# Kernel tuning notes

Measured on AMD Instinct MI355X. Metric: run time of the kernel, lower is better.

Reference implementation:

```python
import jax, jax.numpy as jnp
import numpy as np

H = 1024   # lstm_size
Z = 512    # z_size
E = 32     # subseq_embedding_dim
B = 256    # batch
T = 64     # length


def setup_inputs() -> dict:
    key = jax.random.key(0)
    ks = jax.random.split(key, 16)
    k = 1.0 / np.sqrt(H)  # PyTorch default uniform init bound
    u = lambda kk, shape: jax.random.uniform(kk, shape, jnp.float32, -k, k)
    return {
        "z": jax.random.normal(ks[0], (1, B, Z), jnp.float32),
        "targets": jax.random.normal(ks[1], (T, B, E), jnp.float32),
        "length": T,
        # LSTM layer 0 (input E -> H), gate order i,f,g,o as in PyTorch
        "W_ih0": u(ks[2], (4 * H, E)), "W_hh0": u(ks[3], (4 * H, H)),
        "b_ih0": u(ks[4], (4 * H,)),   "b_hh0": u(ks[5], (4 * H,)),
        # LSTM layer 1 (input H -> H)
        "W_ih1": u(ks[6], (4 * H, H)), "W_hh1": u(ks[7], (4 * H, H)),
        "b_ih1": u(ks[8], (4 * H,)),   "b_hh1": u(ks[9], (4 * H,)),
        # per-layer z -> initial hidden projections
        "Wz0": u(ks[10], (H, Z)), "bz0": u(ks[11], (H,)),
        "Wz1": u(ks[12], (H, Z)), "bz1": u(ks[13], (H,)),
        # output projection H -> E
        "Wp": u(ks[14], (E, H)), "bp": u(ks[15], (E,)),
    }


def _lstm_cell(x, h, c, W_ih, W_hh, b_ih, b_hh):
    # gates: [i, f, g, o] stacked along last dim (PyTorch layout)
    g = x @ W_ih.T + h @ W_hh.T + (b_ih + b_hh)
    i, f, gg, o = jnp.split(g, 4, axis=-1)
    c2 = jax.nn.sigmoid(f) * c + jax.nn.sigmoid(i) * jnp.tanh(gg)
    h2 = jax.nn.sigmoid(o) * jnp.tanh(c2)
    return h2, c2


def reference(z, targets, length, W_ih0, W_hh0, b_ih0, b_hh0,
              W_ih1, W_hh1, b_ih1, b_hh1, Wz0, bz0, Wz1, bz1, Wp, bp):
    batch = z.shape[1]
    emb = targets.shape[-1]
    z0 = z[0]  # (B, Z)
    # initial hidden = tanh(Linear(z)) per layer, initial cell = zeros
    h0 = jnp.tanh(z0 @ Wz0.T + bz0)
    h1 = jnp.tanh(z0 @ Wz1.T + bz1)
    c0 = jnp.zeros_like(h0)
    c1 = jnp.zeros_like(h1)

    # teacher-forced inputs: step 0 is zeros, step t uses targets[t-1] (detached)
    inputs = jnp.concatenate(
        [jnp.zeros((1, batch, emb), targets.dtype),
         jax.lax.stop_gradient(targets[: length - 1])], axis=0)

    def step(carry, x):
        h0, c0, h1, c1 = carry
        h0, c0 = _lstm_cell(x, h0, c0, W_ih0, W_hh0, b_ih0, b_hh0)
        h1, c1 = _lstm_cell(h0, h1, c1, W_ih1, W_hh1, b_ih1, b_hh1)
        out = h1 @ Wp.T + bp  # (B, E)
        return (h0, c0, h1, c1), out

    _, outs = jax.lax.scan(step, (h0, c0, h1, c1), inputs)
    return outs  # (length, B, E) == embedding_outputs
```

## Files before the change

### kernel.cpp

```cpp
#include <hip/hip_runtime.h>

#define TT 64
#define BB 256
#define HH 1024
#define ZZ 512
#define EE 32

#define NKB0 33
#define NKB1 64
#define NKBZ 16
#define NKBP 32

#define SLOTSH ((size_t)(HH / 16) * BB * 16)

typedef __attribute__((ext_vector_type(8))) short short8;
typedef __attribute__((ext_vector_type(4))) float f4;

__device__ __forceinline__ f4 mfma16(short8 a, short8 b, f4 c) {
  return __builtin_amdgcn_mfma_f32_16x16x32_bf16(a, b, c, 0, 0, 0);
}

__device__ __forceinline__ unsigned short f2bf(float f) {
  unsigned u = __builtin_bit_cast(unsigned, f);
  u = u + 0x7fffu + ((u >> 16) & 1u);
  return (unsigned short)(u >> 16);
}

__device__ __forceinline__ float sigm(float x) { return 1.0f / (1.0f + __expf(-x)); }
__device__ __forceinline__ float tanh_f(float x) { return 1.0f - 2.0f / (__expf(2.0f * x) + 1.0f); }

__device__ __forceinline__ short8 ld16(const short* p) { return *(const short8*)p; }

__device__ __forceinline__ short8 ld16_byp(const short* p) {
  union { unsigned long long u[2]; short8 v; } t;
  t.u[0] = __hip_atomic_load((const unsigned long long*)p, __ATOMIC_RELAXED, __HIP_MEMORY_SCOPE_AGENT);
  t.u[1] = __hip_atomic_load((const unsigned long long*)p + 1, __ATOMIC_RELAXED, __HIP_MEMORY_SCOPE_AGENT);
  return t.v;
}

__device__ __forceinline__ void st4_byp(short* p, unsigned v) {
  __hip_atomic_store((unsigned*)p, v, __ATOMIC_RELAXED, __HIP_MEMORY_SCOPE_AGENT);
}

__device__ __forceinline__ void bar_arrive(unsigned* bar, int btid, int jt, unsigned gen) {
  asm volatile("s_waitcnt vmcnt(0)" ::: "memory");
  __syncthreads();
  if (threadIdx.x == 0) {
    unsigned* base = bar + btid * (10 * 32);
    unsigned* leaf = base + (jt >> 3) * 32;
    unsigned prev = __hip_atomic_fetch_add(leaf, 1u, __ATOMIC_RELAXED, __HIP_MEMORY_SCOPE_AGENT);
    if (prev == gen * 8u - 1u) {
      unsigned rp = __hip_atomic_fetch_add(base + 8 * 32, 1u, __ATOMIC_RELAXED, __HIP_MEMORY_SCOPE_AGENT);
      if (rp == gen * 8u - 1u)
        __hip_atomic_store(base + 9 * 32, gen, __ATOMIC_RELAXED, __HIP_MEMORY_SCOPE_AGENT);
    }
  }
}

__device__ __forceinline__ void bar_wait(unsigned* bar, int btid, unsigned gen) {
  if (threadIdx.x == 0) {
    unsigned* flag = bar + btid * (10 * 32) + 9 * 32;
    while (__hip_atomic_load(flag, __ATOMIC_RELAXED, __HIP_MEMORY_SCOPE_AGENT) < gen)
      __builtin_amdgcn_s_sleep(1);
  }
  __syncthreads();
}

__global__ void pack_all(
    const float* __restrict__ z, const float* __restrict__ tg,
    const float* __restrict__ Wih0, const float* __restrict__ Whh0,
    const float* __restrict__ Wih1, const float* __restrict__ Whh1,
    const float* __restrict__ Wz0, const float* __restrict__ Wz1,
    const float* __restrict__ Wp,
    short* __restrict__ W0P, short* __restrict__ W1P,
    short* __restrict__ WzP, short* __restrict__ WpP,
    short* __restrict__ zbf, short* __restrict__ Xbf)
{
  const int N0 = 64 * NKB0 * 4 * 64;
  const int N1 = 64 * NKB1 * 4 * 64;
  const int N2 = 32 * NKBZ * 4 * 64;
  const int N3 = NKBP * 2 * 64;
  const int N4 = (BB * ZZ) / 8;
  const int N5 = (TT * BB * EE) / 8;
  const int TOT = N0 + N1 + N2 + N3 + N4 + N5;
  for (int idx = blockIdx.x * blockDim.x + threadIdx.x; idx < TOT;
       idx += gridDim.x * blockDim.x) {
    int j = idx;
    short8 ov;
    if (j < N0) {
      const int l = j & 63, fc = (j >> 6) & 3, rest = j >> 8;
      const int kb = rest % NKB0, jt = rest / NKB0;
      const int row = fc * HH + jt * 16 + (l & 15);
      const int k0 = kb * 32 + ((l >> 4) * 8);
      #pragma unroll
      for (int i = 0; i < 8; ++i) {
        const int k = k0 + i;
        const float v = (k < HH) ? Whh0[(size_t)row * HH + k]
                                 : Wih0[(size_t)row * EE + (k - HH)];
        ov[i] = (short)f2bf(v);
      }
      *(short8*)(W0P + (size_t)j * 8) = ov;
      continue;
    }
    j -= N0;
    if (j < N1) {
      const int l = j & 63, fc = (j >> 6) & 3, rest = j >> 8;
      const int kb = rest & 63, jt = rest >> 6;
      const int row = fc * HH + jt * 16 + (l & 15);
      const int k0 = kb * 32 + ((l >> 4) * 8);
      #pragma unroll
      for (int i = 0; i < 8; ++i) {
        const int k = k0 + i;
        const float v = (k < HH) ? Wih1[(size_t)row * HH + k]
                                 : Whh1[(size_t)row * HH + (k - HH)];
        ov[i] = (short)f2bf(v);
      }
      *(short8*)(W1P + (size_t)j * 8) = ov;
      continue;
    }
    j -= N1;
    if (j < N2) {
      const int l = j & 63, fc = (j >> 6) & 3, rest = j >> 8;
      const int kb = rest & 15, ct = rest >> 4;
      const int col = ct * 64 + fc * 16 + (l & 15);
      const int lay = col >> 10, ch = col & (HH - 1);
      const int k0 = kb * 32 + ((l >> 4) * 8);
      const float* W = lay ? Wz1 : Wz0;
      #pragma unroll
      for (int i = 0; i < 8; ++i) ov[i] = (short)f2bf(W[(size_t)ch * ZZ + k0 + i]);
      *(short8*)(WzP + (size_t)j * 8) = ov;
      continue;
    }
    j -= N2;
    if (j < N3) {
      const int l = j & 63, fc = (j >> 6) & 1, kb = j >> 7;
      const int e = fc * 16 + (l & 15);
      const int k0 = kb * 32 + ((l >> 4) * 8);
      #pragma unroll
      for (int i = 0; i < 8; ++i) ov[i] = (short)f2bf(Wp[(size_t)e * HH + k0 + i]);
      *(short8*)(WpP + (size_t)j * 8) = ov;
      continue;
    }
    j -= N3;
    if (j < N4) {
      #pragma unroll
      for (int i = 0; i < 8; ++i) ov[i] = (short)f2bf(z[(size_t)j * 8 + i]);
      *(short8*)(zbf + (size_t)j * 8) = ov;
      continue;
    }
    j -= N4;
    {
      const int base = j * 8;
      const int t = base >> 13, rem = base & 8191;
      if (t == 0) {
        #pragma unroll
        for (int i = 0; i < 8; ++i) ov[i] = 0;
      } else {
        #pragma unroll
        for (int i = 0; i < 8; ++i) ov[i] = (short)f2bf(tg[(size_t)(t - 1) * 8192 + rem + i]);
      }
      *(short8*)(Xbf + (size_t)j * 8) = ov;
    }
  }
}

__global__ void __launch_bounds__(256, 1)
init_h(const short* __restrict__ WzP, const short* __restrict__ zbf,
       const float* __restrict__ bz0, const float* __restrict__ bz1,
       short* __restrict__ H0s0, short* __restrict__ H1s0)
{
  __shared__ float red[2][64][66];
  const int wg = blockIdx.x;
  const int btile = (wg >> 5) * 64;
  const int ct = wg & 31;
  const int tid = threadIdx.x;
  const int wv = tid >> 6, ln = tid & 63;
  const int lr = ln & 15, lk = (ln >> 4) * 8, hi4 = (ln >> 4) * 4;

  f4 acc[4][4];
  #pragma unroll
  for (int r = 0; r < 4; ++r)
    #pragma unroll
    for (int c = 0; c < 4; ++c) acc[r][c] = (f4)0.0f;

  #pragma unroll 2
  for (int i = 0; i < 4; ++i) {
    const int kb = wv + i * 4;
    short8 av[4], bv[4];
    const short* ap = zbf + (size_t)(btile + lr) * ZZ + kb * 32 + lk;
    #pragma unroll
    for (int r = 0; r < 4; ++r) av[r] = ld16(ap + (size_t)r * 16 * ZZ);
    const short* bp = WzP + ((size_t)(ct * NKBZ + kb) * 4) * 512 + ln * 8;
    #pragma unroll
    for (int c = 0; c < 4; ++c) bv[c] = ld16(bp + (size_t)c * 512);
    #pragma unroll
    for (int r = 0; r < 4; ++r)
      #pragma unroll
      for (int c = 0; c < 4; ++c) acc[r][c] = mfma16(av[r], bv[c], acc[r][c]);
  }

  if (wv < 2) {
    #pragma unroll
    for (int r = 0; r < 4; ++r)
      #pragma unroll
      for (int c = 0; c < 4; ++c)
        #pragma unroll
        for (int q = 0; q < 4; ++q)
          red[wv][r * 16 + hi4 + q][c * 16 + lr] = acc[r][c][q];
  }
  __syncthreads();
  if (wv >= 2) {
    #pragma unroll
    for (int r = 0; r < 4; ++r)
      #pragma unroll
      for (int c = 0; c < 4; ++c)
        #pragma unroll
        for (int q = 0; q < 4; ++q)
          red[wv - 2][r * 16 + hi4 + q][c * 16 + lr] += acc[r][c][q];
  }
  __syncthreads();

  const int c2 = tid & 63, rr = tid >> 6;
  #pragma unroll
  for (int k = 0; k < 16; ++k) {
    const int r = rr + k * 4;
    const int cg = ct * 64 + c2;
    const int lay = cg >> 10, ch = cg & (HH - 1);
    const float v = tanh_f(red[0][r][c2] + red[1][r][c2] + (lay ? bz1[ch] : bz0[ch]));
    short* dst = lay ? H1s0 : H0s0;
    dst[(size_t)(ch >> 4) * (BB * 16) + (size_t)(btile + r) * 16 + (ch & 15)] = (short)f2bf(v);
  }
}

template <bool BIG>
__global__ void __launch_bounds__(512, 1)
lstm_seq(const short* __restrict__ W0P, const short* __restrict__ W1P,
         const short* __restrict__ Xbf,
         short* __restrict__ H0, short* __restrict__ H1,
         short* __restrict__ H1a,
         const float* __restrict__ bi0, const float* __restrict__ bh0,
         const float* __restrict__ bi1, const float* __restrict__ bh1,
         unsigned* __restrict__ bar)
{
  __shared__ float red[4][64][68];
  const int wg = blockIdx.x;
  const int x = wg & 7;
  const int q = wg >> 3;
  const int jt = x + 8 * (q & 7);
  const int btid = q >> 3;
  const int btile = btid * 64;
  const int tid = threadIdx.x;
  const int wv = tid >> 6, ln = tid & 63;
  const int lr = ln & 15, lk = (ln >> 4) * 8, hi4 = (ln >> 4) * 4;

  const int u = tid & 15;
  const int rbase = tid >> 4;
  const int colg = jt * 16 + u;

  float bs0[4], bs1[4];
  #pragma unroll
  for (int g = 0; g < 4; ++g) {
    bs0[g] = bi0[g * HH + colg] + bh0[g * HH + colg];
    bs1[g] = bi1[g * HH + colg] + bh1[g * HH + colg];
  }

  const short* W0w = W0P + (size_t)jt * NKB0 * 4 * 512;
  const short* W1w = W1P + (size_t)jt * NKB1 * 4 * 512;

  const int aoff = (lk >> 4) * (BB * 16) + (btile + lr) * 16 + (lk & 15);
  const size_t ewi = (size_t)jt * (BB * 16) + u;

  float c0reg[2] = {0.0f, 0.0f}, c1reg[2] = {0.0f, 0.0f};

  for (int t = 0; t < TT; ++t) {
    const short* h0in = H0 + (size_t)(BIG ? t : (t & 1)) * SLOTSH;
    short* h0out      = H0 + (size_t)(BIG ? (t + 1) : ((t + 1) & 1)) * SLOTSH;
    const short* h1in = H1 + (size_t)(BIG ? t : (t & 1)) * SLOTSH;
    short* h1out      = H1 + (size_t)(BIG ? (t + 1) : ((t + 1) & 1)) * SLOTSH;

    f4 acc[4][4];
    #pragma unroll
    for (int r = 0; r < 4; ++r)
      #pragma unroll
      for (int c = 0; c < 4; ++c) acc[r][c] = (f4)0.0f;

    #pragma unroll
    for (int i = 0; i < 4; ++i) {
      const int kb = wv + 8 * i;
      short8 av[4], bv[4];
      const short* ap = h0in + (size_t)kb * 2 * (BB * 16) + aoff;
      #pragma unroll
      for (int r = 0; r < 4; ++r)
        av[r] = BIG ? ld16(ap + r * 256) : ld16_byp(ap + r * 256);
      const short* bp = W0w + (size_t)kb * 4 * 512 + ln * 8;
      #pragma unroll
      for (int c = 0; c < 4; ++c) bv[c] = ld16(bp + (size_t)c * 512);
      #pragma unroll
      for (int r = 0; r < 4; ++r)
        #pragma unroll
        for (int c = 0; c < 4; ++c) acc[r][c] = mfma16(av[r], bv[c], acc[r][c]);
    }

    {
      const short* xbase = Xbf + (size_t)((size_t)t * BB + btile + lr) * EE + lk;
      const short* bp32 = W0w + (size_t)32 * 4 * 512 + ln * 8;
      #pragma unroll
      for (int r = 0; r < 4; ++r)
        #pragma unroll
        for (int c = 0; c < 4; ++c)
          if (((r * 4 + c) >> 1) == wv) {
            const short8 av = ld16(xbase + (size_t)r * 16 * EE);
            const short8 bv = ld16(bp32 + (size_t)c * 512);
            acc[r][c] = mfma16(av, bv, acc[r][c]);
          }
    }

    if (wv < 4) {
      #pragma unroll
      for (int r = 0; r < 4; ++r)
        #pragma unroll
        for (int c = 0; c < 4; ++c)
          *(f4*)&red[wv][c * 16 + lr][r * 16 + hi4] = acc[r][c];
    }
    __syncthreads();
    if (wv >= 4) {
      #pragma unroll
      for (int r = 0; r < 4; ++r)
        #pragma unroll
        for (int c = 0; c < 4; ++c) {
          f4* p = (f4*)&red[wv - 4][c * 16 + lr][r * 16 + hi4];
          f4 v = *p;
          v += acc[r][c];
          *p = v;
        }
    }
    __syncthreads();

    #pragma unroll
    for (int k = 0; k < 2; ++k) {
      const int r = rbase + 32 * k;
      float s[4];
      #pragma unroll
      for (int g = 0; g < 4; ++g)
        s[g] = red[0][g * 16 + u][r] + red[1][g * 16 + u][r]
             + red[2][g * 16 + u][r] + red[3][g * 16 + u][r] + bs0[g];
      const float gi = sigm(s[0]), gf = sigm(s[1]);
      const float gg = tanh_f(s[2]), go = sigm(s[3]);
      c0reg[k] = gf * c0reg[k] + gi * gg;
      const unsigned hv = (unsigned)f2bf(go * tanh_f(c0reg[k]));
      const unsigned ov = (unsigned)__shfl_xor((int)hv, 1, 64);
      if ((tid & 1) == 0)
        st4_byp(h0out + ewi + (size_t)(btile + r) * 16, hv | (ov << 16));
    }

    short8 bv0[4];
    {
      const short* bp0 = W1w + (size_t)wv * 4 * 512 + ln * 8;
      #pragma unroll
      for (int c = 0; c < 4; ++c) bv0[c] = ld16(bp0 + (size_t)c * 512);
    }

    bar_arrive(bar, btid, jt, (unsigned)(t + 1));

    #pragma unroll
    for (int r = 0; r < 4; ++r)
      #pragma unroll
      for (int c = 0; c < 4; ++c) acc[r][c] = (f4)0.0f;

    short8 a1[4][4];
    #pragma unroll
    for (int j = 0; j < 4; ++j) {
      const short* ap = h1in + (size_t)(wv + 8 * j) * 2 * (BB * 16) + aoff;
      #pragma unroll
      for (int r = 0; r < 4; ++r)
        a1[j][r] = BIG ? ld16(ap + r * 256) : ld16_byp(ap + r * 256);
    }
    #pragma unroll
    for (int j = 0; j < 4; ++j) {
      const int kb = wv + 8 * j + 32;
      short8 bv[4];
      const short* bp = W1w + (size_t)kb * 4 * 512 + ln * 8;
      #pragma unroll
      for (int c = 0; c < 4; ++c) bv[c] = ld16(bp + (size_t)c * 512);
      #pragma unroll
      for (int r = 0; r < 4; ++r)
        #pragma unroll
        for (int c = 0; c < 4; ++c) acc[r][c] = mfma16(a1[j][r], bv[c], acc[r][c]);
    }

    bar_wait(bar, btid, (unsigned)(t + 1));

    #pragma unroll
    for (int i = 0; i < 4; ++i) {
      const int kb = wv + 8 * i;
      short8 av[4], bv[4];
      const short* ap = h0out + (size_t)kb * 2 * (BB * 16) + aoff;
      #pragma unroll
      for (int r = 0; r < 4; ++r)
        av[r] = BIG ? ld16(ap + r * 256) : ld16_byp(ap + r * 256);
      if (i == 0) {
        #pragma unroll
        for (int c = 0; c < 4; ++c) bv[c] = bv0[c];
      } else {
        const short* bp = W1w + (size_t)kb * 4 * 512 + ln * 8;
        #pragma unroll
        for (int c = 0; c < 4; ++c) bv[c] = ld16(bp + (size_t)c * 512);
      }
      #pragma unroll
      for (int r = 0; r < 4; ++r)
        #pragma unroll
        for (int c = 0; c < 4; ++c) acc[r][c] = mfma16(av[r], bv[c], acc[r][c]);
    }

    if (wv < 4) {
      #pragma unroll
      for (int r = 0; r < 4; ++r)
        #pragma unroll
        for (int c = 0; c < 4; ++c)
          *(f4*)&red[wv][c * 16 + lr][r * 16 + hi4] = acc[r][c];
    }
    __syncthreads();
    if (wv >= 4) {
      #pragma unroll
      for (int r = 0; r < 4; ++r)
        #pragma unroll
        for (int c = 0; c < 4; ++c) {
          f4* p = (f4*)&red[wv - 4][c * 16 + lr][r * 16 + hi4];
          f4 v = *p;
          v += acc[r][c];
          *p = v;
        }
    }
    __syncthreads();

    #pragma unroll
    for (int k = 0; k < 2; ++k) {
      const int r = rbase + 32 * k;
      float s[4];
      #pragma unroll
      for (int g = 0; g < 4; ++g)
        s[g] = red[0][g * 16 + u][r] + red[1][g * 16 + u][r]
             + red[2][g * 16 + u][r] + red[3][g * 16 + u][r] + bs1[g];
      const float gi = sigm(s[0]), gf = sigm(s[1]);
      const float gg = tanh_f(s[2]), go = sigm(s[3]);
      c1reg[k] = gf * c1reg[k] + gi * gg;
      const unsigned hv = (unsigned)f2bf(go * tanh_f(c1reg[k]));
      const unsigned ov = (unsigned)__shfl_xor((int)hv, 1, 64);
      if ((tid & 1) == 0) {
        const size_t ci = ewi + (size_t)(btile + r) * 16;
        const unsigned pv = hv | (ov << 16);
        st4_byp(h1out + ci, pv);
        if (!BIG) st4_byp(H1a + (size_t)t * SLOTSH + ci, pv);
      }
    }
    __syncthreads();
  }
}

__global__ void __launch_bounds__(256, 1)
proj(const short* __restrict__ H1a, const short* __restrict__ WpP,
     const float* __restrict__ bp, float* __restrict__ out)
{
  __shared__ float red[2][64][34];
  const int rt = blockIdx.x * 64;
  const int tslot = rt >> 8;
  const int rb = rt & 255;
  const int tid = threadIdx.x;
  const int wv = tid >> 6, ln = tid & 63;
  const int lr = ln & 15, lk = (ln >> 4) * 8, hi4 = (ln >> 4) * 4;

  const short* base = H1a + (size_t)tslot * SLOTSH;
  const int aoff = (lk >> 4) * (BB * 16) + (rb + lr) * 16 + (lk & 15);

  f4 acc[4][2];
  #pragma unroll
  for (int r = 0; r < 4; ++r)
    #pragma unroll
    for (int c = 0; c < 2; ++c) acc[r][c] = (f4)0.0f;

  #pragma unroll 2
  for (int i = 0; i < 8; ++i) {
    const int kb = wv + i * 4;
    short8 av[4], bv[2];
    const short* ap = base + (size_t)kb * 2 * (BB * 16) + aoff;
    #pragma unroll
    for (int r = 0; r < 4; ++r) av[r] = ld16(ap + r * 256);
    const short* bq = WpP + (size_t)kb * 2 * 512 + ln * 8;
    #pragma unroll
    for (int c = 0; c < 2; ++c) bv[c] = ld16(bq + (size_t)c * 512);
    #pragma unroll
    for (int r = 0; r < 4; ++r)
      #pragma unroll
      for (int c = 0; c < 2; ++c) acc[r][c] = mfma16(av[r], bv[c], acc[r][c]);
  }

  if (wv < 2) {
    #pragma unroll
    for (int r = 0; r < 4; ++r)
      #pragma unroll
      for (int c = 0; c < 2; ++c)
        #pragma unroll
        for (int q = 0; q < 4; ++q)
          red[wv][r * 16 + hi4 + q][c * 16 + lr] = acc[r][c][q];
  }
  __syncthreads();
  if (wv >= 2) {
    #pragma unroll
    for (int r = 0; r < 4; ++r)
      #pragma unroll
      for (int c = 0; c < 2; ++c)
        #pragma unroll
        for (int q = 0; q < 4; ++q)
          red[wv - 2][r * 16 + hi4 + q][c * 16 + lr] += acc[r][c][q];
  }
  __syncthreads();

  const int ce = tid & 31, rr = tid >> 5;
  #pragma unroll
  for (int k = 0; k < 8; ++k) {
    const int r = rr + k * 8;
    out[(size_t)(rt + r) * EE + ce] = red[0][r][ce] + red[1][r][ce] + bp[ce];
  }
}

extern "C" void kernel_launch(void* const* d_in, const int* in_sizes, int n_in,
                              void* d_out, int out_size, void* d_ws, size_t ws_size,
                              hipStream_t stream) {
  const float* z    = (const float*)d_in[0];
  const float* tg   = (const float*)d_in[1];
  const float* Wih0 = (const float*)d_in[3];
  const float* Whh0 = (const float*)d_in[4];
  const float* bi0  = (const float*)d_in[5];
  const float* bh0  = (const float*)d_in[6];
  const float* Wih1 = (const float*)d_in[7];
  const float* Whh1 = (const float*)d_in[8];
  const float* bi1  = (const float*)d_in[9];
  const float* bh1  = (const float*)d_in[10];
  const float* Wz0  = (const float*)d_in[11];
  const float* bz0  = (const float*)d_in[12];
  const float* Wz1  = (const float*)d_in[13];
  const float* bz1  = (const float*)d_in[14];
  const float* Wp   = (const float*)d_in[15];
  const float* bpv  = (const float*)d_in[16];

  char* ws = (char*)d_ws;
  size_t off = 0;
  unsigned* bar = (unsigned*)(ws + off); off += 8192;
  short* W0P  = (short*)(ws + off); off += (size_t)64 * NKB0 * 4 * 512 * 2;
  short* W1P  = (short*)(ws + off); off += (size_t)64 * NKB1 * 4 * 512 * 2;
  short* WzP  = (short*)(ws + off); off += (size_t)32 * NKBZ * 4 * 512 * 2;
  short* WpP  = (short*)(ws + off); off += (size_t)NKBP * 2 * 512 * 2;
  short* zbf  = (short*)(ws + off); off += (size_t)BB * ZZ * 2;
  short* Xbf  = (short*)(ws + off); off += (size_t)TT * BB * EE * 2;

  const size_t seqB = (size_t)(TT + 1) * SLOTSH * 2;
  const size_t need_big = off + 2 * seqB;
  const size_t need_small = off + 2 * ((size_t)2 * SLOTSH * 2) + (size_t)TT * SLOTSH * 2;
  const bool big = (ws_size >= need_big);

  if (ws_size < need_small) return;

  hipMemsetAsync(bar, 0, 8192, stream);

  pack_all<<<dim3(1024), dim3(256), 0, stream>>>(z, tg, Wih0, Whh0, Wih1, Whh1,
                                                 Wz0, Wz1, Wp,
                                                 W0P, W1P, WzP, WpP, zbf, Xbf);
  if (big) {
    short* H0seq = (short*)(ws + off);
    short* H1seq = (short*)(ws + off + seqB);
    init_h<<<dim3(128), dim3(256), 0, stream>>>(WzP, zbf, bz0, bz1, H0seq, H1seq);
    lstm_seq<true><<<dim3(256), dim3(512), 0, stream>>>(W0P, W1P, Xbf, H0seq, H1seq,
                                                        (short*)nullptr,
                                                        bi0, bh0, bi1, bh1, bar);
    proj<<<dim3(256), dim3(256), 0, stream>>>(H1seq + SLOTSH, WpP, bpv, (float*)d_out);
  } else {
    short* H0pp = (short*)(ws + off);
    short* H1pp = H0pp + 2 * SLOTSH;
    short* H1a  = H1pp + 2 * SLOTSH;
    init_h<<<dim3(128), dim3(256), 0, stream>>>(WzP, zbf, bz0, bz1, H0pp, H1pp);
    lstm_seq<false><<<dim3(256), dim3(512), 0, stream>>>(W0P, W1P, Xbf, H0pp, H1pp,
                                                         H1a,
                                                         bi0, bh0, bi1, bh1, bar);
    proj<<<dim3(256), dim3(256), 0, stream>>>(H1a, WpP, bpv, (float*)d_out);
  }
}
```

Before: 868.5 us.

## Replace tree barrier with flat counters and reuse h0 fragments across steps

Replaces the two-level atomic tree barrier with two flat per-batch-tile counters: one marks the mid-step h0 write and one marks the end of step. An added wait on the end counter keeps the double-buffered h1/h0 slots from being overwritten early. The h0 A-fragments loaded for the layer-1 input matmul are kept in registers (a0sav) and reused as the layer-0 recurrent operand in the next step, which removes a redundant global reload. The cost is more register pressure from holding 16 short8 values across the loop, plus 64-way contention on a single atomic counter.

```diff
diff --git a/kernel.cpp b/kernel.cpp
--- a/kernel.cpp
+++ b/kernel.cpp
@@ -42,28 +42,12 @@
   __hip_atomic_store((unsigned*)p, v, __ATOMIC_RELAXED, __HIP_MEMORY_SCOPE_AGENT);
 }
 
-__device__ __forceinline__ void bar_arrive(unsigned* bar, int btid, int jt, unsigned gen) {
-  asm volatile("s_waitcnt vmcnt(0)" ::: "memory");
-  __syncthreads();
-  if (threadIdx.x == 0) {
-    unsigned* base = bar + btid * (10 * 32);
-    unsigned* leaf = base + (jt >> 3) * 32;
-    unsigned prev = __hip_atomic_fetch_add(leaf, 1u, __ATOMIC_RELAXED, __HIP_MEMORY_SCOPE_AGENT);
-    if (prev == gen * 8u - 1u) {
-      unsigned rp = __hip_atomic_fetch_add(base + 8 * 32, 1u, __ATOMIC_RELAXED, __HIP_MEMORY_SCOPE_AGENT);
-      if (rp == gen * 8u - 1u)
-        __hip_atomic_store(base + 9 * 32, gen, __ATOMIC_RELAXED, __HIP_MEMORY_SCOPE_AGENT);
-    }
-  }
-}
-
-__device__ __forceinline__ void bar_wait(unsigned* bar, int btid, unsigned gen) {
-  if (threadIdx.x == 0) {
-    unsigned* flag = bar + btid * (10 * 32) + 9 * 32;
-    while (__hip_atomic_load(flag, __ATOMIC_RELAXED, __HIP_MEMORY_SCOPE_AGENT) < gen)
-      __builtin_amdgcn_s_sleep(1);
-  }
-  __syncthreads();
+__device__ __forceinline__ void ctr_inc(unsigned* c) {
+  __hip_atomic_fetch_add(c, 1u, __ATOMIC_RELAXED, __HIP_MEMORY_SCOPE_AGENT);
+}
+__device__ __forceinline__ void ctr_wait(unsigned* c, unsigned target) {
+  while (__hip_atomic_load(c, __ATOMIC_RELAXED, __HIP_MEMORY_SCOPE_AGENT) < target)
+    __builtin_amdgcn_s_sleep(1);
 }
 
 __global__ void pack_all(
@@ -257,6 +241,9 @@
   const int rbase = tid >> 4;
   const int colg = jt * 16 + u;
 
+  unsigned* cntMid = bar + btid * 64;
+  unsigned* cntEnd = bar + btid * 64 + 32;
+
   float bs0[4], bs1[4];
   #pragma unroll
   for (int g = 0; g < 4; ++g) {
@@ -272,8 +259,16 @@
 
   float c0reg[2] = {0.0f, 0.0f}, c1reg[2] = {0.0f, 0.0f};
 
+  short8 a0sav[4][4];
+  #pragma unroll
+  for (int i = 0; i < 4; ++i) {
+    const short* ap = H0 + (size_t)(wv + 8 * i) * 2 * (BB * 16) + aoff;
+    #pragma unroll
+    for (int r = 0; r < 4; ++r)
+      a0sav[i][r] = BIG ? ld16(ap + r * 256) : ld16_byp(ap + r * 256);
+  }
+
   for (int t = 0; t < TT; ++t) {
-    const short* h0in = H0 + (size_t)(BIG ? t : (t & 1)) * SLOTSH;
     short* h0out      = H0 + (size_t)(BIG ? (t + 1) : ((t + 1) & 1)) * SLOTSH;
     const short* h1in = H1 + (size_t)(BIG ? t : (t & 1)) * SLOTSH;
     short* h1out      = H1 + (size_t)(BIG ? (t + 1) : ((t + 1) & 1)) * SLOTSH;
@@ -287,18 +282,14 @@
     #pragma unroll
     for (int i = 0; i < 4; ++i) {
       const int kb = wv + 8 * i;
-      short8 av[4], bv[4];
-      const short* ap = h0in + (size_t)kb * 2 * (BB * 16) + aoff;
-      #pragma unroll
-      for (int r = 0; r < 4; ++r)
-        av[r] = BIG ? ld16(ap + r * 256) : ld16_byp(ap + r * 256);
+      short8 bv[4];
       const short* bp = W0w + (size_t)kb * 4 * 512 + ln * 8;
       #pragma unroll
       for (int c = 0; c < 4; ++c) bv[c] = ld16(bp + (size_t)c * 512);
       #pragma unroll
       for (int r = 0; r < 4; ++r)
         #pragma unroll
-        for (int c = 0; c < 4; ++c) acc[r][c] = mfma16(av[r], bv[c], acc[r][c]);
+        for (int c = 0; c < 4; ++c) acc[r][c] = mfma16(a0sav[i][r], bv[c], acc[r][c]);
     }
 
     {
@@ -360,7 +351,12 @@
       for (int c = 0; c < 4; ++c) bv0[c] = ld16(bp0 + (size_t)c * 512);
     }
 
-    bar_arrive(bar, btid, jt, (unsigned)(t + 1));
+    asm volatile("s_waitcnt vmcnt(0)" ::: "memory");
+    __syncthreads();
+    if (tid == 0) ctr_inc(cntMid);
+
+    if (tid == 0) ctr_wait(cntEnd, (unsigned)t * 64u);
+    __syncthreads();
 
     #pragma unroll
     for (int r = 0; r < 4; ++r)
@@ -388,16 +384,17 @@
         for (int c = 0; c < 4; ++c) acc[r][c] = mfma16(a1[j][r], bv[c], acc[r][c]);
     }
 
-    bar_wait(bar, btid, (unsigned)(t + 1));
+    if (tid == 0) ctr_wait(cntMid, (unsigned)(t + 1) * 64u);
+    __syncthreads();
 
     #pragma unroll
     for (int i = 0; i < 4; ++i) {
       const int kb = wv + 8 * i;
-      short8 av[4], bv[4];
+      short8 bv[4];
       const short* ap = h0out + (size_t)kb * 2 * (BB * 16) + aoff;
       #pragma unroll
       for (int r = 0; r < 4; ++r)
-        av[r] = BIG ? ld16(ap + r * 256) : ld16_byp(ap + r * 256);
+        a0sav[i][r] = BIG ? ld16(ap + r * 256) : ld16_byp(ap + r * 256);
       if (i == 0) {
         #pragma unroll
         for (int c = 0; c < 4; ++c) bv[c] = bv0[c];
@@ -409,7 +406,7 @@
       #pragma unroll
       for (int r = 0; r < 4; ++r)
         #pragma unroll
-        for (int c = 0; c < 4; ++c) acc[r][c] = mfma16(av[r], bv[c], acc[r][c]);
+        for (int c = 0; c < 4; ++c) acc[r][c] = mfma16(a0sav[i][r], bv[c], acc[r][c]);
     }
 
     if (wv < 4) {
@@ -454,6 +451,7 @@
       }
     }
     __syncthreads();
+    if (tid == 0) ctr_inc(cntEnd);
   }
 }
 
```

After: 1.105 ms. 27.2% more time.
